# Optimization experiments

Measured on AMD Instinct MI355X. Metric: run time of the kernel, lower is better.

The kernel has to match this reference:

```python
import jax, jax.numpy as jnp
import numpy as np
import math

B, K, M, D = 8192, 16, 16, 256
LAMBDA_FGW = 0.5
TAU_KL = 0.1
N_OUTER = 5
N_SINKHORN = 10


def setup_inputs() -> dict:
    key = jax.random.key(0)
    ks = jax.random.split(key, 8)
    return {
        'slots_q': jax.random.normal(ks[0], (B, K, D), jnp.float32),
        'slots_r': jax.random.normal(ks[1], (B, M, D), jnp.float32),
        'mask_q': jnp.ones((B, K), jnp.float32),
        'mask_r': jnp.ones((B, M), jnp.float32),
        'centroids_q': jax.random.uniform(ks[2], (B, K, 2), jnp.float32),
        'centroids_r': jax.random.uniform(ks[3], (B, M, 2), jnp.float32),
        'W1': jax.random.normal(ks[4], (D, D), jnp.float32) * 0.05,
        'b1': jnp.zeros((D,), jnp.float32),
        'W2': jax.random.normal(ks[5], (D, D), jnp.float32) * 0.05,
        'b2': jnp.zeros((D,), jnp.float32),
        'log_eps': jnp.asarray(math.log(0.05), jnp.float32),
    }


def _pdist(a, b):
    # ||a_i - b_j||, clamped like torch: clamp(sumsq, 1e-6).sqrt()
    d2 = (jnp.sum(a * a, -1)[:, :, None] + jnp.sum(b * b, -1)[:, None, :]
          - 2.0 * jnp.einsum('bkd,bmd->bkm', a, b))
    return jnp.sqrt(jnp.clip(d2, 1e-6, None))


def reference(slots_q, slots_r, mask_q, mask_r, centroids_q, centroids_r,
              W1, b1, W2, b2, log_eps):
    proj = lambda x: jax.nn.relu(x @ W1.T + b1) @ W2.T + b2
    pq, pr = proj(slots_q), proj(slots_r)
    C = _pdist(pq, pr)                      # [B,K,M]
    Sq = _pdist(centroids_q, centroids_q)   # [B,K,K]
    Sr = _pdist(centroids_r, centroids_r)   # [B,M,M]

    mu = mask_q / (jnp.sum(mask_q, -1, keepdims=True) + 1e-8)
    nu = mask_r / (jnp.sum(mask_r, -1, keepdims=True) + 1e-8)
    T = mu[:, :, None] * nu[:, None, :]

    eps = jnp.clip(jnp.exp(log_eps), 0.01, 0.5)
    rho = TAU_KL / (TAU_KL + eps)
    log_mu = jnp.log(jnp.clip(mu, 1e-8, None))
    log_nu = jnpp = jnp.log(jnp.clip(nu, 1e-8, None))
    Sq2, Sr2 = Sq * Sq, Sr * Sr

    C_fgw = C
    for _ in range(N_OUTER):
        t1 = jnp.einsum('bkl,bl->bk', Sq2, T.sum(2))[:, :, None]
        t2 = jnp.einsum('bm,bmn->bn', T.sum(1), Sr2)[:, None, :]
        t3 = -2.0 * jnp.einsum('bkl,blm,bmn->bkn', Sq, T, Sr)
        L_gw = t1 + t2 + t3
        C_fgw = (1.0 - LAMBDA_FGW) * C + LAMBDA_FGW * L_gw
        log_K = -C_fgw / eps
        log_u = jnp.zeros_like(mu)
        log_v = jnp.zeros_like(nu)
        for _ in range(N_SINKHORN):
            log_u = rho * (log_mu - jax.nn.logsumexp(log_K + log_v[:, None, :], axis=2))
            log_v = rho * (log_nu - jax.nn.logsumexp(log_K + log_u[:, :, None], axis=1))
        T = jnp.exp(log_u[:, :, None] + log_K + log_v[:, None, :])

    cost = jnp.sum(T * C_fgw, axis=(-1, -2))
    return (jax.nn.sigmoid(-cost), T, C, cost)
```

## Files before the change

### kernel.cpp

```cpp
#include <hip/hip_runtime.h>


#define OFF_T   8192
#define OFF_C   2105344
#define OFF_CST 4202496

typedef float  f32x4  __attribute__((ext_vector_type(4)));
typedef float  f32x16 __attribute__((ext_vector_type(16)));
typedef short  s16x8  __attribute__((ext_vector_type(8)));

__device__ __forceinline__ unsigned short f2bf(float f) {
  unsigned int u = __float_as_uint(f);
  u += 0x7FFFu + ((u >> 16) & 1u);
  return (unsigned short)(u >> 16);
}
__device__ __forceinline__ float bf2f(unsigned short h) {
  return __uint_as_float(((unsigned int)h) << 16);
}

template <int CTRL>
__device__ __forceinline__ float dpp_add(float x) {
  return x + __int_as_float(__builtin_amdgcn_update_dpp(
      0, __float_as_int(x), CTRL, 0xf, 0xf, true));
}
template <int CTRL>
__device__ __forceinline__ float dpp_max(float x) {
  return fmaxf(x, __int_as_float(__builtin_amdgcn_update_dpp(
      0, __float_as_int(x), CTRL, 0xf, 0xf, true)));
}
__device__ __forceinline__ float row16_sum(float x) {
  x = dpp_add<0xB1>(x);  x = dpp_add<0x4E>(x);
  x = dpp_add<0x124>(x); x = dpp_add<0x128>(x);
  return x;
}
__device__ __forceinline__ float row16_max(float x) {
  x = dpp_max<0xB1>(x);  x = dpp_max<0x4E>(x);
  x = dpp_max<0x124>(x); x = dpp_max<0x128>(x);
  return x;
}
__device__ __forceinline__ float xor16_add(float x) {
  return x + __int_as_float(__builtin_amdgcn_ds_swizzle(__float_as_int(x), 0x401F));
}
__device__ __forceinline__ float xor16_max(float x) {
  return fmaxf(x, __int_as_float(__builtin_amdgcn_ds_swizzle(__float_as_int(x), 0x401F)));
}
__device__ __forceinline__ float xor32_add(float x) { return x + __shfl_xor(x, 32); }
__device__ __forceinline__ float xor32_max(float x) { return fmaxf(x, __shfl_xor(x, 32)); }

__global__ __launch_bounds__(256, 1)
void prep_w32(const float* __restrict__ W1, const float* __restrict__ W2,
              unsigned int* __restrict__ wh)
{
  const int fid  = blockIdx.x * 256 + threadIdx.x;
  const int l    = fid >> 13;
  const int s    = (fid >> 9) & 15;
  const int cg   = (fid >> 6) & 7;
  const int lane = fid & 63;
  const int col  = cg * 32 + (lane & 31);
  const int k0   = s * 16 + ((lane >> 5) << 3);
  const float* W = l ? W2 : W1;
  const float* src = W + ((size_t)col << 8) + k0;
  float4 a = *(const float4*)src;
  float4 b = *(const float4*)(src + 4);
  float f[8] = {a.x, a.y, a.z, a.w, b.x, b.y, b.z, b.w};
  unsigned int uh[4];
  #pragma unroll
  for (int i = 0; i < 4; ++i)
    uh[i] = (unsigned)f2bf(f[2*i]) | ((unsigned)f2bf(f[2*i+1]) << 16);
  uint4 vh = {uh[0], uh[1], uh[2], uh[3]};
  ((uint4*)wh)[fid] = vh;
}

__global__ __launch_bounds__(512, 2)
void fgw_proj(const float* __restrict__ g_q,  const float* __restrict__ g_r,
              const unsigned short* __restrict__ wh,
              const float* __restrict__ g_b1, const float* __restrict__ g_b2,
              float* __restrict__ g_out)
{
  __shared__ __align__(16) float smemf[8448];
  char* sm = (char*)smemf;
  float* normL = smemf + 8192;
  const int bId0 = blockIdx.x * 2;
  const int tid  = threadIdx.x;
  const int lane = tid & 63, wid = tid >> 6;
  const int cl   = lane & 31, half = lane >> 5;
  const int b    = wid & 1,  c = wid >> 1;
  const int cg0  = (c << 1), cg1 = (c << 1) + 1;

  #pragma unroll
  for (int j = 0; j < 4; ++j) {
    int idx = (j << 9) + tid;
    int bb  = idx >> 10;
    int t   = idx & 1023;
    int r   = t >> 6;
    int sg  = t & 63;
    int off = ((sg << 3) ^ ((r & 15) << 4));
    char* xb = sm + bb * 16384;
    const f32x4* xq = (const f32x4*)(g_q + (size_t)(bId0 + bb) * 4096 + (r << 8) + (sg << 2));
    const f32x4* xr = (const f32x4*)(g_r + (size_t)(bId0 + bb) * 4096 + (r << 8) + (sg << 2));
    f32x4 v0 = __builtin_nontemporal_load(xq);
    f32x4 v1 = __builtin_nontemporal_load(xr);
    {
      unsigned int* ph = (unsigned int*)(xb + r * 512 + off);
      ph[0] = (unsigned)f2bf(v0[0]) | ((unsigned)f2bf(v0[1]) << 16);
      ph[1] = (unsigned)f2bf(v0[2]) | ((unsigned)f2bf(v0[3]) << 16);
    }
    {
      unsigned int* ph = (unsigned int*)(xb + (16 + r) * 512 + off);
      ph[0] = (unsigned)f2bf(v1[0]) | ((unsigned)f2bf(v1[1]) << 16);
      ph[1] = (unsigned)f2bf(v1[2]) | ((unsigned)f2bf(v1[3]) << 16);
    }
  }
  __syncthreads();

  char* xb = sm + b * 16384;

  for (int layer = 0; layer < 2; ++layer) {
    f32x16 acc0, acc1;
    #pragma unroll
    for (int i = 0; i < 16; ++i) { acc0[i] = 0.f; acc1[i] = 0.f; }

    const float* bl_ = layer ? g_b2 : g_b1;
    #pragma unroll
    for (int ks = 0; ks < 16; ++ks) {
      const size_t f0 = ((((size_t)layer * 16 + ks) * 8 + cg0) * 64 + lane) * 8;
      s16x8 bh0 = *(const s16x8*)(wh + f0);
      s16x8 bh1 = *(const s16x8*)(wh + f0 + 512);
      const int aoff = (((ks << 5) + (half << 4)) ^ ((cl & 15) << 4));
      s16x8 a0 = *(const s16x8*)(xb + cl * 512 + aoff);
      acc0 = __builtin_amdgcn_mfma_f32_32x32x16_bf16(a0, bh0, acc0, 0, 0, 0);
      acc1 = __builtin_amdgcn_mfma_f32_32x32x16_bf16(a0, bh1, acc1, 0, 0, 0);
    }
    __syncthreads();

    const float bv0  = bl_[(cg0 << 5) + cl];
    const float bv1  = bl_[(cg1 << 5) + cl];
    const int colb0  = (((cg0 << 5) + cl) << 1);
    const int colb1  = (((cg1 << 5) + cl) << 1);

    if (layer == 0) {
      #pragma unroll
      for (int reg = 0; reg < 16; ++reg) {
        int rr   = (reg & 3) + ((reg >> 2) << 3) + (half << 2);
        int off0 = colb0 ^ ((rr & 15) << 4);
        int off1 = colb1 ^ ((rr & 15) << 4);
        *(unsigned short*)(xb + rr * 512 + off0) = f2bf(fmaxf(acc0[reg] + bv0, 0.f));
        *(unsigned short*)(xb + rr * 512 + off1) = f2bf(fmaxf(acc1[reg] + bv1, 0.f));
      }
      __syncthreads();
    } else {
      #pragma unroll
      for (int reg = 0; reg < 16; ++reg) {
        int rr   = (reg & 3) + ((reg >> 2) << 3) + (half << 2);
        int off0 = colb0 ^ ((rr & 15) << 4);
        int off1 = colb1 ^ ((rr & 15) << 4);
        float p0 = acc0[reg] + bv0, p1 = acc1[reg] + bv1;
        float s = xor16_add(row16_sum(p0 * p0 + p1 * p1));
        if (cl == 0) normL[(b * 4 + c) * 32 + rr] = s;
        *(unsigned short*)(xb + rr * 512 + off0) = f2bf(p0);
        *(unsigned short*)(xb + rr * 512 + off1) = f2bf(p1);
      }
      __syncthreads();
    }
  }

  const int fr = lane & 15, fg = lane >> 4;
  f32x4 accG = {0.f, 0.f, 0.f, 0.f};
  const int bbG = wid & 1, quad = wid >> 1;
  {
    char* xg = sm + bbG * 16384;
    #pragma unroll
    for (int kk = 0; kk < 2; ++kk) {
      int ks16 = (quad << 1) + kk;
      int koff = ((ks16 << 6) + (fg << 4)) ^ ((fr & 15) << 4);
      s16x8 aq = *(const s16x8*)(xg +        fr * 512 + koff);
      s16x8 br = *(const s16x8*)(xg + (16 + fr) * 512 + koff);
      accG = __builtin_amdgcn_mfma_f32_16x16x32_bf16(aq, br, accG, 0, 0, 0);
    }
  }
  __syncthreads();
  float* Gp = smemf;
  #pragma unroll
  for (int j = 0; j < 4; ++j)
    Gp[(bbG * 4 + quad) * 256 + ((fg << 2) + j) * 16 + fr] = accG[j];
  __syncthreads();

  {
    const int bbC = tid >> 8;
    const int t2  = tid & 255;
    const int tk  = t2 >> 4, tm = t2 & 15;
    float Gv = Gp[(bbC*4+0)*256 + t2] + Gp[(bbC*4+1)*256 + t2]
             + Gp[(bbC*4+2)*256 + t2] + Gp[(bbC*4+3)*256 + t2];
    float nq = 0.f, nr = 0.f;
    #pragma unroll
    for (int cc = 0; cc < 4; ++cc) {
      nq += normL[(bbC*4+cc)*32 + tk];
      nr += normL[(bbC*4+cc)*32 + 16 + tm];
    }
    float Cv = sqrtf(fmaxf(nq + nr - 2.0f * Gv, 1e-6f));
    __builtin_nontemporal_store(Cv, g_out + OFF_C + (size_t)(bId0 + bbC) * 256 + t2);
  }
}

__global__ __launch_bounds__(256, 8)
void fgw_sink(const float* __restrict__ g_mq, const float* __restrict__ g_mr,
              const float* __restrict__ g_cq, const float* __restrict__ g_cr,
              const float* __restrict__ g_leps, float* __restrict__ g_out)
{
  __shared__ __align__(16) float sk[4 * 1088];
  const int tid  = threadIdx.x, lane = tid & 63, w = tid >> 6;
  const int batch = blockIdx.x * 4 + w;
  const int m = lane & 15, g = lane >> 4;
  float* L     = sk + w * 1088;
  float* SqL   = L;        float* SrL   = L + 320;
  float* TtL   = L + 640;  float* M1L   = L + 640;
  float* lmuL  = L + 960;  float* muL   = L + 976;
  float* cqxL  = L + 992;  float* cqyL  = L + 1008;
  float* crxL  = L + 1024; float* cryL  = L + 1040;
  float* trowL = L + 1056; float* tcolL = L + 1072;

  float mqv = g_mq[(size_t)batch * 16 + m];
  float mrv = g_mr[(size_t)batch * 16 + m];
  float mu_m = mqv / (row16_sum(mqv) + 1e-8f);
  float nu_m = mrv / (row16_sum(mrv) + 1e-8f);
  float lmu_m = __logf(fmaxf(mu_m, 1e-8f));
  float lnu_m = __logf(fmaxf(nu_m, 1e-8f));
  float cqx_m = g_cq[(size_t)batch * 32 + 2 * m];
  float cqy_m = g_cq[(size_t)batch * 32 + 2 * m + 1];
  float crx_m = g_cr[(size_t)batch * 32 + 2 * m];
  float cry_m = g_cr[(size_t)batch * 32 + 2 * m + 1];
  if (g == 0) {
    lmuL[m] = lmu_m;  muL[m] = mu_m;
    cqxL[m] = cqx_m;  cqyL[m] = cqy_m;
    crxL[m] = crx_m;  cryL[m] = cry_m;
  }
  f32x4 lmu_j = *(const f32x4*)(lmuL + 4 * g);
  f32x4 mu_j  = *(const f32x4*)(muL  + 4 * g);
  f32x4 cqxj  = *(const f32x4*)(cqxL + 4 * g);
  f32x4 cqyj  = *(const f32x4*)(cqyL + 4 * g);
  f32x4 crxj  = *(const f32x4*)(crxL + 4 * g);
  f32x4 cryj  = *(const f32x4*)(cryL + 4 * g);

  float Sq2r[4], Sr2r[4];
  #pragma unroll
  for (int j = 0; j < 4; ++j) {
    float dx = cqxj[j] - cqx_m, dy = cqyj[j] - cqy_m;
    float d2 = fmaxf(dx * dx + dy * dy, 1e-6f);
    SqL[(4 * g + j) * 20 + m] = sqrtf(d2);
    Sq2r[j] = d2;
    float ex = crxj[j] - crx_m, ey = cryj[j] - cry_m;
    float e2 = fmaxf(ex * ex + ey * ey, 1e-6f);
    SrL[(4 * g + j) * 20 + m] = sqrtf(e2);
    Sr2r[j] = e2;
  }

  float C_[4];
  const float* Cp = g_out + OFF_C + (size_t)batch * 256;
  #pragma unroll
  for (int j = 0; j < 4; ++j) C_[j] = Cp[(4 * g + j) * 16 + m];
  float eps = fminf(fmaxf(__expf(g_leps[0]), 0.01f), 0.5f);
  const float inv_eps = 1.0f / eps;
  const float rho = 0.1f / (0.1f + eps);
  float rlmu[4];
  #pragma unroll
  for (int j = 0; j < 4; ++j) rlmu[j] = rho * lmu_j[j];
  const float rlnu = rho * lnu_m;
  float T_[4];
  #pragma unroll
  for (int j = 0; j < 4; ++j) T_[j] = mu_j[j] * nu_m;

  float Cf[4], logK[4], KM[4], Mx[4], u_[4], v = 0.f;

  for (int it = 0; it < 5; ++it) {
    float trow_j[4];
    #pragma unroll
    for (int j = 0; j < 4; ++j) trow_j[j] = row16_sum(T_[j]);
    float tc = xor32_add(xor16_add(T_[0] + T_[1] + T_[2] + T_[3]));
    if (m == 0) { f32x4 tv = {trow_j[0], trow_j[1], trow_j[2], trow_j[3]};
                  *(f32x4*)(trowL + 4 * g) = tv; }
    if (g == 0) tcolL[m] = tc;
    { f32x4 tv = {T_[0], T_[1], T_[2], T_[3]};
      *(f32x4*)(TtL + m * 20 + 4 * g) = tv; }

    float trow_m = trowL[m];
    float t1_[4];
    #pragma unroll
    for (int j = 0; j < 4; ++j) t1_[j] = row16_sum(Sq2r[j] * trow_m);
    f32x4 tcv = *(const f32x4*)(tcolL + 4 * g);
    float p2 = tcv[0] * Sr2r[0] + tcv[1] * Sr2r[1] + tcv[2] * Sr2r[2] + tcv[3] * Sr2r[3];
    float t2_ = xor32_add(xor16_add(p2));

    float M1r[4] = {0.f, 0.f, 0.f, 0.f};
    #pragma unroll
    for (int l = 0; l < 16; ++l) {
      f32x4 t4 = *(const f32x4*)(TtL + l * 20 + 4 * g);
      float srv = SrL[l * 20 + m];
      M1r[0] += t4[0] * srv; M1r[1] += t4[1] * srv;
      M1r[2] += t4[2] * srv; M1r[3] += t4[3] * srv;
    }
    #pragma unroll
    for (int j = 0; j < 4; ++j) M1L[(4 * g + j) * 20 + m] = M1r[j];
    float t3_[4] = {0.f, 0.f, 0.f, 0.f};
    #pragma unroll
    for (int l = 0; l < 16; ++l) {
      f32x4 sq4 = *(const f32x4*)(SqL + l * 20 + 4 * g);
      float m1v = M1L[l * 20 + m];
      t3_[0] += sq4[0] * m1v; t3_[1] += sq4[1] * m1v;
      t3_[2] += sq4[2] * m1v; t3_[3] += sq4[3] * m1v;
    }

    #pragma unroll
    for (int j = 0; j < 4; ++j) {
      float lgw = t1_[j] + t2_ - 2.0f * t3_[j];
      Cf[j]   = 0.5f * C_[j] + 0.5f * lgw;
      logK[j] = -inv_eps * Cf[j];
      Mx[j]   = row16_max(logK[j]);
      KM[j]   = logK[j] - Mx[j];
    }

    v = 0.f;
    #pragma unroll 1
    for (int s = 0; s < 10; ++s) {
      #pragma unroll
      for (int j = 0; j < 4; ++j) {
        float sj = row16_sum(__expf(KM[j] + v));
        u_[j] = rlmu[j] - rho * (Mx[j] + __logf(sj));
      }
      float x0 = logK[0] + u_[0], x1 = logK[1] + u_[1];
      float x2 = logK[2] + u_[2], x3 = logK[3] + u_[3];
      float mx = fmaxf(fmaxf(x0, x1), fmaxf(x2, x3));
      mx = xor32_max(xor16_max(mx));
      float ss = __expf(x0 - mx) + __expf(x1 - mx) + __expf(x2 - mx) + __expf(x3 - mx);
      ss = xor32_add(xor16_add(ss));
      v = rlnu - rho * (mx + __logf(ss));
    }
    #pragma unroll
    for (int j = 0; j < 4; ++j) T_[j] = __expf(u_[j] + logK[j] + v);
  }

  float cp = T_[0] * Cf[0] + T_[1] * Cf[1] + T_[2] * Cf[2] + T_[3] * Cf[3];
  cp = xor32_add(xor16_add(row16_sum(cp)));
  float* To = g_out + OFF_T + (size_t)batch * 256;
  #pragma unroll
  for (int j = 0; j < 4; ++j)
    __builtin_nontemporal_store(T_[j], To + (4 * g + j) * 16 + m);
  if (lane == 0) {
    g_out[batch] = 1.0f / (1.0f + __expf(cp));
    g_out[OFF_CST + batch] = cp;
  }
}

extern "C" void kernel_launch(void* const* d_in, const int* in_sizes, int n_in,
                              void* d_out, int out_size, void* d_ws, size_t ws_size,
                              hipStream_t stream) {
  (void)in_sizes; (void)n_in; (void)out_size; (void)ws_size;
  unsigned int*   wh32 = (unsigned int*)d_ws;
  unsigned short* wh   = (unsigned short*)wh32;

  prep_w32<<<dim3(64), dim3(256), 0, stream>>>(
      (const float*)d_in[6], (const float*)d_in[8], wh32);
  fgw_proj<<<dim3(4096), dim3(512), 0, stream>>>(
      (const float*)d_in[0], (const float*)d_in[1], wh,
      (const float*)d_in[7], (const float*)d_in[9], (float*)d_out);
  fgw_sink<<<dim3(2048), dim3(256), 0, stream>>>(
      (const float*)d_in[2], (const float*)d_in[3],
      (const float*)d_in[4], (const float*)d_in[5],
      (const float*)d_in[10], (float*)d_out);
}
```

Before: 235.6 us.

## Share weight fragment across both batches per wave and use hardware bf16 pack

```diff
diff --git a/kernel.cpp b/kernel.cpp
--- a/kernel.cpp
+++ b/kernel.cpp
@@ -9,13 +9,15 @@
 typedef float  f32x16 __attribute__((ext_vector_type(16)));
 typedef short  s16x8  __attribute__((ext_vector_type(8)));
 
-__device__ __forceinline__ unsigned short f2bf(float f) {
-  unsigned int u = __float_as_uint(f);
-  u += 0x7FFFu + ((u >> 16) & 1u);
-  return (unsigned short)(u >> 16);
-}
-__device__ __forceinline__ float bf2f(unsigned short h) {
-  return __uint_as_float(((unsigned int)h) << 16);
+__device__ __forceinline__ unsigned int cvt_pk_bf16(float lo, float hi) {
+  unsigned int r;
+  asm("v_cvt_pk_bf16_f32 %0, %1, %2" : "=v"(r) : "v"(lo), "v"(hi));
+  return r;
+}
+__device__ __forceinline__ unsigned short cvt_bf16(float x) {
+  unsigned int r;
+  asm("v_cvt_pk_bf16_f32 %0, %1, %2" : "=v"(r) : "v"(x), "v"(x));
+  return (unsigned short)r;
 }
 
 template <int CTRL>
@@ -62,12 +64,8 @@
   const float* src = W + ((size_t)col << 8) + k0;
   float4 a = *(const float4*)src;
   float4 b = *(const float4*)(src + 4);
-  float f[8] = {a.x, a.y, a.z, a.w, b.x, b.y, b.z, b.w};
-  unsigned int uh[4];
-  #pragma unroll
-  for (int i = 0; i < 4; ++i)
-    uh[i] = (unsigned)f2bf(f[2*i]) | ((unsigned)f2bf(f[2*i+1]) << 16);
-  uint4 vh = {uh[0], uh[1], uh[2], uh[3]};
+  uint4 vh = {cvt_pk_bf16(a.x, a.y), cvt_pk_bf16(a.z, a.w),
+              cvt_pk_bf16(b.x, b.y), cvt_pk_bf16(b.z, b.w)};
   ((uint4*)wh)[fid] = vh;
 }
 
@@ -77,15 +75,13 @@
               const float* __restrict__ g_b1, const float* __restrict__ g_b2,
               float* __restrict__ g_out)
 {
-  __shared__ __align__(16) float smemf[8448];
+  __shared__ __align__(16) float smemf[8704];
   char* sm = (char*)smemf;
   float* normL = smemf + 8192;
   const int bId0 = blockIdx.x * 2;
   const int tid  = threadIdx.x;
   const int lane = tid & 63, wid = tid >> 6;
   const int cl   = lane & 31, half = lane >> 5;
-  const int b    = wid & 1,  c = wid >> 1;
-  const int cg0  = (c << 1), cg1 = (c << 1) + 1;
 
   #pragma unroll
   for (int j = 0; j < 4; ++j) {
@@ -102,18 +98,16 @@
     f32x4 v1 = __builtin_nontemporal_load(xr);
     {
       unsigned int* ph = (unsigned int*)(xb + r * 512 + off);
-      ph[0] = (unsigned)f2bf(v0[0]) | ((unsigned)f2bf(v0[1]) << 16);
-      ph[1] = (unsigned)f2bf(v0[2]) | ((unsigned)f2bf(v0[3]) << 16);
+      ph[0] = cvt_pk_bf16(v0[0], v0[1]);
+      ph[1] = cvt_pk_bf16(v0[2], v0[3]);
     }
     {
       unsigned int* ph = (unsigned int*)(xb + (16 + r) * 512 + off);
-      ph[0] = (unsigned)f2bf(v1[0]) | ((unsigned)f2bf(v1[1]) << 16);
-      ph[1] = (unsigned)f2bf(v1[2]) | ((unsigned)f2bf(v1[3]) << 16);
+      ph[0] = cvt_pk_bf16(v1[0], v1[1]);
+      ph[1] = cvt_pk_bf16(v1[2], v1[3]);
     }
   }
   __syncthreads();
-
-  char* xb = sm + b * 16384;
 
   for (int layer = 0; layer < 2; ++layer) {
     f32x16 acc0, acc1;
@@ -123,42 +117,42 @@
     const float* bl_ = layer ? g_b2 : g_b1;
     #pragma unroll
     for (int ks = 0; ks < 16; ++ks) {
-      const size_t f0 = ((((size_t)layer * 16 + ks) * 8 + cg0) * 64 + lane) * 8;
-      s16x8 bh0 = *(const s16x8*)(wh + f0);
-      s16x8 bh1 = *(const s16x8*)(wh + f0 + 512);
+      const size_t f0 = ((((size_t)layer * 16 + ks) * 8 + wid) * 64 + lane) * 8;
+      s16x8 bh = *(const s16x8*)(wh + f0);
       const int aoff = (((ks << 5) + (half << 4)) ^ ((cl & 15) << 4));
-      s16x8 a0 = *(const s16x8*)(xb + cl * 512 + aoff);
-      acc0 = __builtin_amdgcn_mfma_f32_32x32x16_bf16(a0, bh0, acc0, 0, 0, 0);
-      acc1 = __builtin_amdgcn_mfma_f32_32x32x16_bf16(a0, bh1, acc1, 0, 0, 0);
+      s16x8 a0 = *(const s16x8*)(sm +         cl * 512 + aoff);
+      s16x8 a1 = *(const s16x8*)(sm + 16384 + cl * 512 + aoff);
+      acc0 = __builtin_amdgcn_mfma_f32_32x32x16_bf16(a0, bh, acc0, 0, 0, 0);
+      acc1 = __builtin_amdgcn_mfma_f32_32x32x16_bf16(a1, bh, acc1, 0, 0, 0);
     }
     __syncthreads();
 
-    const float bv0  = bl_[(cg0 << 5) + cl];
-    const float bv1  = bl_[(cg1 << 5) + cl];
-    const int colb0  = (((cg0 << 5) + cl) << 1);
-    const int colb1  = (((cg1 << 5) + cl) << 1);
+    const float bv  = bl_[(wid << 5) + cl];
+    const int  colb = (((wid << 5) + cl) << 1);
 
     if (layer == 0) {
       #pragma unroll
       for (int reg = 0; reg < 16; ++reg) {
-        int rr   = (reg & 3) + ((reg >> 2) << 3) + (half << 2);
-        int off0 = colb0 ^ ((rr & 15) << 4);
-        int off1 = colb1 ^ ((rr & 15) << 4);
-        *(unsigned short*)(xb + rr * 512 + off0) = f2bf(fmaxf(acc0[reg] + bv0, 0.f));
-        *(unsigned short*)(xb + rr * 512 + off1) = f2bf(fmaxf(acc1[reg] + bv1, 0.f));
+        int rr  = (reg & 3) + ((reg >> 2) << 3) + (half << 2);
+        int off = colb ^ ((rr & 15) << 4);
+        *(unsigned short*)(sm +         rr * 512 + off) = cvt_bf16(fmaxf(acc0[reg] + bv, 0.f));
+        *(unsigned short*)(sm + 16384 + rr * 512 + off) = cvt_bf16(fmaxf(acc1[reg] + bv, 0.f));
       }
       __syncthreads();
     } else {
       #pragma unroll
       for (int reg = 0; reg < 16; ++reg) {
-        int rr   = (reg & 3) + ((reg >> 2) << 3) + (half << 2);
-        int off0 = colb0 ^ ((rr & 15) << 4);
-        int off1 = colb1 ^ ((rr & 15) << 4);
-        float p0 = acc0[reg] + bv0, p1 = acc1[reg] + bv1;
-        float s = xor16_add(row16_sum(p0 * p0 + p1 * p1));
-        if (cl == 0) normL[(b * 4 + c) * 32 + rr] = s;
-        *(unsigned short*)(xb + rr * 512 + off0) = f2bf(p0);
-        *(unsigned short*)(xb + rr * 512 + off1) = f2bf(p1);
+        int rr  = (reg & 3) + ((reg >> 2) << 3) + (half << 2);
+        int off = colb ^ ((rr & 15) << 4);
+        float p0 = acc0[reg] + bv, p1 = acc1[reg] + bv;
+        float s0 = xor16_add(row16_sum(p0 * p0));
+        float s1 = xor16_add(row16_sum(p1 * p1));
+        if (cl == 0) {
+          normL[(0 * 8 + wid) * 32 + rr] = s0;
+          normL[(1 * 8 + wid) * 32 + rr] = s1;
+        }
+        *(unsigned short*)(sm +         rr * 512 + off) = cvt_bf16(p0);
+        *(unsigned short*)(sm + 16384 + rr * 512 + off) = cvt_bf16(p1);
       }
       __syncthreads();
     }
@@ -193,9 +187,9 @@
              + Gp[(bbC*4+2)*256 + t2] + Gp[(bbC*4+3)*256 + t2];
     float nq = 0.f, nr = 0.f;
     #pragma unroll
-    for (int cc = 0; cc < 4; ++cc) {
-      nq += normL[(bbC*4+cc)*32 + tk];
-      nr += normL[(bbC*4+cc)*32 + 16 + tm];
+    for (int cc = 0; cc < 8; ++cc) {
+      nq += normL[(bbC*8+cc)*32 + tk];
+      nr += normL[(bbC*8+cc)*32 + 16 + tm];
     }
     float Cv = sqrtf(fmaxf(nq + nr - 2.0f * Gv, 1e-6f));
     __builtin_nontemporal_store(Cv, g_out + OFF_C + (size_t)(bId0 + bbC) * 256 + t2);
```

New measurement: 241.4 us. 2.5% more time.
